# Kernel optimization log

Measured on AMD Instinct MI355X. Metric: run time of the kernel, lower is better.

Reference implementation:

```python
import jax, jax.numpy as jnp
import numpy as np

EPS = 1e-8  # torch.nn.CosineSimilarity default eps


def setup_inputs() -> dict:
    key = jax.random.key(0)
    mapping = jax.random.normal(key, (8192, 512), dtype=jnp.float32)
    return {"mapping": mapping}


def reference(mapping) -> jnp.ndarray:
    # Pairwise cosine distance: 1 - (x_i . x_j) / max(||x_i||*||x_j||, eps)
    # Efficient form: single N x D GEMM + outer product of norms
    dots = mapping @ mapping.T                      # [N, N]
    norms = jnp.linalg.norm(mapping, axis=-1)       # [N]
    denom = jnp.maximum(norms[:, None] * norms[None, :], EPS)
    return 1.0 - dots / denom
```

## Files before the change

kernel.cpp:

```cpp
#include <hip/hip_runtime.h>

typedef __attribute__((ext_vector_type(8))) short bf16x8;
typedef __attribute__((ext_vector_type(8))) unsigned short u16x8;
typedef __attribute__((ext_vector_type(4))) float f32x4;

__device__ __forceinline__ unsigned short f2bf(float f) {
    unsigned int u = __float_as_uint(f);
    u += 0x7fffu + ((u >> 16) & 1u);
    return (unsigned short)(u >> 16);
}

__global__ __launch_bounds__(256) void normalize_rows(
    const float* __restrict__ X, unsigned short* __restrict__ Y) {
    const int wave = threadIdx.x >> 6;
    const int lane = threadIdx.x & 63;
    const long row = (long)blockIdx.x * 4 + wave;

    const float4* xr = (const float4*)(X + row * 512);
    float4 a = xr[lane * 2];
    float4 b = xr[lane * 2 + 1];

    float s = a.x * a.x + a.y * a.y + a.z * a.z + a.w * a.w
            + b.x * b.x + b.y * b.y + b.z * b.z + b.w * b.w;
#pragma unroll
    for (int off = 32; off; off >>= 1) s += __shfl_xor(s, off, 64);

    const float inv = rsqrtf(s);

    u16x8 o;
    o[0] = f2bf(a.x * inv); o[1] = f2bf(a.y * inv);
    o[2] = f2bf(a.z * inv); o[3] = f2bf(a.w * inv);
    o[4] = f2bf(b.x * inv); o[5] = f2bf(b.y * inv);
    o[6] = f2bf(b.z * inv); o[7] = f2bf(b.w * inv);
    ((u16x8*)(Y + row * 512))[lane] = o;
}

#define GLDS16(g, l)                                                         \
    __builtin_amdgcn_global_load_lds(                                        \
        (const __attribute__((address_space(1))) void*)(g),                  \
        (__attribute__((address_space(3))) void*)(l), 16, 0, 0)

__global__ __launch_bounds__(256) void cosdist_gemm(
    const unsigned short* __restrict__ Y, float* __restrict__ out) {
    constexpr int N = 8192, K = 512, BM = 128, BK = 32;

    __shared__ __align__(16) short As[BM * BK];
    __shared__ __align__(16) short Bs[BM * BK];

    const int tid  = threadIdx.x;
    const int lane = tid & 63;
    const int wave = tid >> 6;
    const int wr = wave >> 1, wc = wave & 1;
    const int bm = blockIdx.x * BM;
    const int bn = blockIdx.y * BM;

    f32x4 acc[4][4] = {};

    const int c0 = tid, c1 = tid + 256;
    const unsigned short* Ag0 = Y + (size_t)(bm + (c0 >> 2)) * K + ((c0 & 3) << 3);
    const unsigned short* Ag1 = Y + (size_t)(bm + (c1 >> 2)) * K + ((c1 & 3) << 3);
    const unsigned short* Bg0 = Y + (size_t)(bn + (c0 >> 2)) * K + ((c0 & 3) << 3);
    const unsigned short* Bg1 = Y + (size_t)(bn + (c1 >> 2)) * K + ((c1 & 3) << 3);
    short* Al0 = As + c0 * 8;
    short* Al1 = As + c1 * 8;
    short* Bl0 = Bs + c0 * 8;
    short* Bl1 = Bs + c1 * 8;

    const int frow = lane & 15;
    const int fk   = (lane >> 4) << 3;

    for (int k0 = 0; k0 < K; k0 += BK) {
        GLDS16(Ag0 + k0, Al0);
        GLDS16(Ag1 + k0, Al1);
        GLDS16(Bg0 + k0, Bl0);
        GLDS16(Bg1 + k0, Bl1);
        __syncthreads();

        bf16x8 af[4], bfr[4];
#pragma unroll
        for (int t = 0; t < 4; ++t) {
            af[t]  = *(const bf16x8*)&As[(wr * 64 + t * 16 + frow) * BK + fk];
            bfr[t] = *(const bf16x8*)&Bs[(wc * 64 + t * 16 + frow) * BK + fk];
        }
#pragma unroll
        for (int mt = 0; mt < 4; ++mt)
#pragma unroll
            for (int nt = 0; nt < 4; ++nt)
                acc[mt][nt] = __builtin_amdgcn_mfma_f32_16x16x32_bf16(
                    af[mt], bfr[nt], acc[mt][nt], 0, 0, 0);
        __syncthreads();
    }

    const int crow0 = wr * 64 + ((lane >> 4) << 2);
    const int ccol0 = wc * 64 + (lane & 15);
#pragma unroll
    for (int mt = 0; mt < 4; ++mt)
#pragma unroll
        for (int nt = 0; nt < 4; ++nt)
#pragma unroll
            for (int r = 0; r < 4; ++r) {
                const int row = bm + crow0 + mt * 16 + r;
                const int col = bn + ccol0 + nt * 16;
                out[(size_t)row * N + col] = 1.0f - acc[mt][nt][r];
            }
}

extern "C" void kernel_launch(void* const* d_in, const int* in_sizes, int n_in,
                              void* d_out, int out_size, void* d_ws, size_t ws_size,
                              hipStream_t stream) {
    const float* X = (const float*)d_in[0];
    float* out = (float*)d_out;
    unsigned short* Y = (unsigned short*)d_ws;

    const int D = 512;
    const int N = in_sizes[0] / D;

    normalize_rows<<<N / 4, 256, 0, stream>>>(X, Y);
    dim3 grid(N / 128, N / 128);
    cosdist_gemm<<<grid, 256, 0, stream>>>(Y, out);
}
```

Measured before the change: 321.8 us.

## Exploit symmetry: compute upper-triangular tiles and write both transposed outputs

Launches only the upper-triangular tile pairs of the Gram matrix, decoding the tile indices from a linear block id with a sqrt-based inverse triangular formula. Each off-diagonal tile is written twice, once at its own position and once transposed, and the transposed store uses 16-byte vector writes. This roughly halves the MFMA work and the operand loads. The cost is unchanged total output traffic, now with scattered scalar stores on the non-transposed side, and the kernel is likely bound by writing the 256MB output anyway.

```diff
diff --git a/kernel.cpp b/kernel.cpp
--- a/kernel.cpp
+++ b/kernel.cpp
@@ -40,19 +40,27 @@
         (const __attribute__((address_space(1))) void*)(g),                  \
         (__attribute__((address_space(3))) void*)(l), 16, 0, 0)
 
-__global__ __launch_bounds__(256) void cosdist_gemm(
+__global__ __launch_bounds__(256) void cosdist_gemm_sym(
     const unsigned short* __restrict__ Y, float* __restrict__ out) {
     constexpr int N = 8192, K = 512, BM = 128, BK = 32;
+    constexpr int NTI = N / BM;
+    constexpr int A2 = 2 * NTI + 1;
 
     __shared__ __align__(16) short As[BM * BK];
     __shared__ __align__(16) short Bs[BM * BK];
+
+    const int p = blockIdx.x;
+    int bi = (int)floorf((A2 - sqrtf((float)(A2 * A2) - 8.0f * (float)p)) * 0.5f);
+    while ((bi + 1) * (A2 - (bi + 1)) / 2 <= p) ++bi;
+    while (bi * (A2 - bi) / 2 > p) --bi;
+    const int bj = bi + (p - bi * (A2 - bi) / 2);
+    const int bm = bi * BM;
+    const int bn = bj * BM;
 
     const int tid  = threadIdx.x;
     const int lane = tid & 63;
     const int wave = tid >> 6;
     const int wr = wave >> 1, wc = wave & 1;
-    const int bm = blockIdx.x * BM;
-    const int bn = blockIdx.y * BM;
 
     f32x4 acc[4][4] = {};
 
@@ -93,16 +101,26 @@
 
     const int crow0 = wr * 64 + ((lane >> 4) << 2);
     const int ccol0 = wc * 64 + (lane & 15);
+    const bool offdiag = (bm != bn);
+
 #pragma unroll
     for (int mt = 0; mt < 4; ++mt)
 #pragma unroll
-        for (int nt = 0; nt < 4; ++nt)
+        for (int nt = 0; nt < 4; ++nt) {
+            f32x4 v;
 #pragma unroll
-            for (int r = 0; r < 4; ++r) {
-                const int row = bm + crow0 + mt * 16 + r;
-                const int col = bn + ccol0 + nt * 16;
-                out[(size_t)row * N + col] = 1.0f - acc[mt][nt][r];
+            for (int r = 0; r < 4; ++r) v[r] = 1.0f - acc[mt][nt][r];
+            const int row = bm + crow0 + mt * 16;
+            const int col = bn + ccol0 + nt * 16;
+
+            *(f32x4*)&out[(size_t)col * N + row] = v;
+
+            if (offdiag) {
+#pragma unroll
+                for (int r = 0; r < 4; ++r)
+                    out[(size_t)(row + r) * N + col] = v[r];
             }
+        }
 }
 
 extern "C" void kernel_launch(void* const* d_in, const int* in_sizes, int n_in,
@@ -116,6 +134,8 @@
     const int N = in_sizes[0] / D;
 
     normalize_rows<<<N / 4, 256, 0, stream>>>(X, Y);
-    dim3 grid(N / 128, N / 128);
-    cosdist_gemm<<<grid, 256, 0, stream>>>(Y, out);
+
+    const int nt = N / 128;
+    const int ntiles = nt * (nt + 1) / 2;
+    cosdist_gemm_sym<<<ntiles, 256, 0, stream>>>(Y, out);
 }
```

New measurement: 348.1 us. +8.2%, slower.
